# Optimization experiments

Hardware: AMD Instinct MI355X
Metric: run time of the kernel (lower is better)

The kernel has to match this reference:

```python
import jax, jax.numpy as jnp
import numpy as np

B, L, D_MODEL, H, D_QKV = 4, 2048, 1024, 16, 64
SCALE = float(D_MODEL) ** 0.5  # note: source scales by sqrt(d_model), not sqrt(d_qkv)


def setup_inputs() -> dict:
    key = jax.random.key(0)
    ks = jax.random.split(key, 6)
    xavier_qkv = (2.0 / (D_MODEL + D_QKV)) ** 0.5
    xavier_fc = (2.0 / (H * D_QKV + D_MODEL)) ** 0.5
    return {
        "x": jax.random.normal(ks[0], (B, L, D_MODEL), dtype=jnp.float32),
        "mask": jnp.ones((B, L), dtype=jnp.int32),
        "w_q": jax.random.normal(ks[1], (H, D_MODEL, D_QKV), dtype=jnp.float32) * xavier_qkv,
        "w_k": jax.random.normal(ks[2], (H, D_MODEL, D_QKV), dtype=jnp.float32) * xavier_qkv,
        "w_v": jax.random.normal(ks[3], (H, D_MODEL, D_QKV), dtype=jnp.float32) * xavier_qkv,
        "fc_w": jax.random.normal(ks[4], (D_MODEL, H * D_QKV), dtype=jnp.float32) * xavier_fc,
        "fc_b": jnp.zeros((D_MODEL,), dtype=jnp.float32),
    }


def reference(x, mask, w_q, w_k, w_v, fc_w, fc_b):
    # x: [B, L, M]; per-head projections via einsum, as in the source
    q = jnp.einsum('blm,hmd->blhd', x, w_q)
    k = jnp.einsum('blm,hmd->blhd', x, w_k)
    v = jnp.einsum('blm,hmd->blhd', x, w_v)
    scores = jnp.einsum('blhd,bkhd->bhlk', q, k)  # [B, H, L, L]
    m = mask[:, None, None, :]  # unsqueeze(1).unsqueeze(2)
    scores = jnp.where(m == 0, jnp.asarray(-1e9, scores.dtype), scores)
    logits = jax.nn.softmax(scores / SCALE, axis=3)
    # Faithful to source einsum 'bhlk,blhd->blhd' (k is summed out of logits only)
    out = jnp.einsum('bhlk,blhd->blhd', logits, v)
    out = out.reshape(x.shape[0], x.shape[1], H * D_QKV)
    return out @ fc_w.T + fc_b
```

## Files before the change

### kernel.cpp

```cpp
#include <hip/hip_runtime.h>
#include <hip/hip_bf16.h>


typedef __attribute__((ext_vector_type(8))) short bf16x8;
typedef __attribute__((ext_vector_type(4))) float f32x4;

__device__ __forceinline__ f32x4 mfma16(bf16x8 a, bf16x8 b, f32x4 c) {
  return __builtin_amdgcn_mfma_f32_16x16x32_bf16(a, b, c, 0, 0, 0);
}

__device__ __forceinline__ unsigned short f2b(float f) {
  unsigned int u = __builtin_bit_cast(unsigned int, f);
  return (unsigned short)((u + 0x7fffu + ((u >> 16) & 1u)) >> 16);
}

__device__ __forceinline__ bf16x8 cvt8(float4 a, float4 b) {
  bf16x8 r;
  r[0] = (short)f2b(a.x); r[1] = (short)f2b(a.y); r[2] = (short)f2b(a.z); r[3] = (short)f2b(a.w);
  r[4] = (short)f2b(b.x); r[5] = (short)f2b(b.y); r[6] = (short)f2b(b.z); r[7] = (short)f2b(b.w);
  return r;
}

__device__ __forceinline__ void gld_lds16(const void* g, void* l) {
  __builtin_amdgcn_global_load_lds((const __attribute__((address_space(1))) unsigned int*)g,
                                   (__attribute__((address_space(3))) unsigned int*)l, 16, 0, 0);
}

__global__ __launch_bounds__(256) void prep(const float* __restrict__ x,
                                            const float* __restrict__ wv,
                                            const float* __restrict__ fcw,
                                            unsigned short* __restrict__ xb,
                                            unsigned short* __restrict__ wcT) {
  int bid = blockIdx.x, t = threadIdx.x;
  int wid = t >> 6, lane = t & 63, l16 = lane & 15, quad = lane >> 4;

  if (bid < 256) {
    int wr = wid >> 1, wc = wid & 1;
    int row0 = (bid >> 4) * 64 + wr * 32;
    int col0 = (bid & 15) * 64 + wc * 32;
    f32x4 acc[2][2];
#pragma unroll
    for (int a = 0; a < 2; a++)
#pragma unroll
      for (int b = 0; b < 2; b++) acc[a][b] = (f32x4){0.f, 0.f, 0.f, 0.f};

    float4 A0[2][2], B0[2][2];
#define LOADK(kk, Ad, Bd)                                                            \
    {                                                                                \
      int h_ = (kk) >> 6, d_ = (kk) & 63;                                            \
      _Pragma("unroll")                                                              \
      for (int rt = 0; rt < 2; rt++) {                                               \
        const float* pa = fcw + (row0 + rt * 16 + l16) * 1024 + (kk);                \
        Ad[rt][0] = *reinterpret_cast<const float4*>(pa);                            \
        Ad[rt][1] = *reinterpret_cast<const float4*>(pa + 4);                        \
      }                                                                              \
      _Pragma("unroll")                                                              \
      for (int ct = 0; ct < 2; ct++) {                                               \
        const float* pb = wv + h_ * 65536 + (col0 + ct * 16 + l16) * 64 + d_;        \
        Bd[ct][0] = *reinterpret_cast<const float4*>(pb);                            \
        Bd[ct][1] = *reinterpret_cast<const float4*>(pb + 4);                        \
      }                                                                              \
    }
    LOADK(quad * 8, A0, B0);
    for (int k0 = 0; k0 < 1024; k0 += 32) {
      float4 A1[2][2], B1[2][2];
      if (k0 < 992) LOADK(k0 + 32 + quad * 8, A1, B1);
      bf16x8 af[2], bfr[2];
#pragma unroll
      for (int rt = 0; rt < 2; rt++) af[rt] = cvt8(A0[rt][0], A0[rt][1]);
#pragma unroll
      for (int ct = 0; ct < 2; ct++) bfr[ct] = cvt8(B0[ct][0], B0[ct][1]);
#pragma unroll
      for (int rt = 0; rt < 2; rt++)
#pragma unroll
        for (int ct = 0; ct < 2; ct++) acc[rt][ct] = mfma16(af[rt], bfr[ct], acc[rt][ct]);
#pragma unroll
      for (int a = 0; a < 2; a++)
#pragma unroll
        for (int b = 0; b < 2; b++) { A0[a][b] = A1[a][b]; B0[a][b] = B1[a][b]; }
    }
#undef LOADK
#pragma unroll
    for (int rt = 0; rt < 2; rt++)
#pragma unroll
      for (int ct = 0; ct < 2; ct++) {
        int j0 = row0 + rt * 16 + quad * 4;
        int m = col0 + ct * 16 + l16;
#pragma unroll
        for (int r = 0; r < 4; r++) wcT[(j0 + r) * 1024 + m] = f2b(acc[rt][ct][r]);
      }
  } else {
    int base0 = (bid - 256) << 15;
#pragma unroll
    for (int i = 0; i < 16; i++) {
      int idx = base0 + i * 2048 + t * 8;
      float4 a = *reinterpret_cast<const float4*>(x + idx);
      float4 b = *reinterpret_cast<const float4*>(x + idx + 4);
      *reinterpret_cast<bf16x8*>(xb + idx) = cvt8(a, b);
    }
  }
}

__global__ __launch_bounds__(256, 4) void final_gemm(const unsigned short* __restrict__ xb,
                                                     const unsigned short* __restrict__ wcT,
                                                     const float* __restrict__ fcb,
                                                     float* __restrict__ out) {
  __shared__ __align__(16) unsigned short As[2 * 128 * 32];
  __shared__ __align__(16) unsigned short Bs[2 * 64 * 32];
  int t = threadIdx.x, wid = t >> 6, lane = t & 63, l16 = lane & 15, quad = lane >> 4;
  int wr = wid >> 1, wc = wid & 1;
  int row0 = (blockIdx.x >> 4) * 128;
  int col0 = (blockIdx.x & 15) * 64;

  int w4 = wid * 4, w2 = wid * 2;
  const unsigned short* Ap[4];
  const unsigned short* Bp[2];
#pragma unroll
  for (int j = 0; j < 4; j++) {
    int blk = w4 + j, s = blk >> 3;
    int row = (blk & 7) * 16 + (lane >> 2), kq = lane & 3;
    Ap[j] = xb + (row0 + row) * 1024 + s * 32 + kq * 8;
  }
#pragma unroll
  for (int j = 0; j < 2; j++) {
    int blk = w2 + j, s = blk >> 2;
    int row = (blk & 3) * 16 + (lane >> 2), kq = lane & 3;
    Bp[j] = wcT + (col0 + row) * 1024 + s * 32 + kq * 8;
  }

  f32x4 acc[4][2];
#pragma unroll
  for (int rt = 0; rt < 4; rt++)
#pragma unroll
    for (int ct = 0; ct < 2; ct++) acc[rt][ct] = (f32x4){0.f, 0.f, 0.f, 0.f};

  for (int k0 = 0; k0 < 1024; k0 += 64) {
    __syncthreads();
#pragma unroll
    for (int j = 0; j < 4; j++) gld_lds16(Ap[j] + k0, &As[(w4 + j) * 512 + lane * 8]);
#pragma unroll
    for (int j = 0; j < 2; j++) gld_lds16(Bp[j] + k0, &Bs[(w2 + j) * 512 + lane * 8]);
    __syncthreads();
#pragma unroll
    for (int s = 0; s < 2; s++) {
      bf16x8 af[4], bfr[2];
#pragma unroll
      for (int rt = 0; rt < 4; rt++)
        af[rt] = *reinterpret_cast<const bf16x8*>(&As[s * 4096 + (wr * 64 + rt * 16 + l16) * 32 + quad * 8]);
#pragma unroll
      for (int ct = 0; ct < 2; ct++)
        bfr[ct] = *reinterpret_cast<const bf16x8*>(&Bs[s * 2048 + (wc * 32 + ct * 16 + l16) * 32 + quad * 8]);
#pragma unroll
      for (int rt = 0; rt < 4; rt++)
#pragma unroll
        for (int ct = 0; ct < 2; ct++)
          acc[rt][ct] = mfma16(af[rt], bfr[ct], acc[rt][ct]);
    }
  }

#pragma unroll
  for (int ct = 0; ct < 2; ct++) {
    int j = col0 + wc * 32 + ct * 16 + l16;
    float bias = fcb[j];
#pragma unroll
    for (int rt = 0; rt < 4; rt++) {
      int i0 = row0 + wr * 64 + rt * 16 + quad * 4;
      f32x4 a = acc[rt][ct];
#pragma unroll
      for (int r = 0; r < 4; r++) out[(i0 + r) * 1024 + j] = a[r] + bias;
    }
  }
}

extern "C" void kernel_launch(void* const* d_in, const int* in_sizes, int n_in,
                              void* d_out, int out_size, void* d_ws, size_t ws_size,
                              hipStream_t stream) {
  const float* x   = (const float*)d_in[0];
  const float* wv  = (const float*)d_in[4];
  const float* fcw = (const float*)d_in[5];
  const float* fcb = (const float*)d_in[6];
  float* out = (float*)d_out;

  char* ws = (char*)d_ws;
  unsigned short* xb  = (unsigned short*)(ws);
  unsigned short* wcT = (unsigned short*)(ws + 16777216);

  prep<<<512, 256, 0, stream>>>(x, wv, fcw, xb, wcT);
  final_gemm<<<1024, 256, 0, stream>>>(xb, wcT, fcb, out);
}
```

Before: 151.1 us.

## Stage weight-fold GEMM tiles through swizzled LDS and widen conversion grid

After: 133.5 us. -11.6%, faster.

```diff
diff --git a/kernel.cpp b/kernel.cpp
--- a/kernel.cpp
+++ b/kernel.cpp
@@ -31,69 +31,100 @@
                                             const float* __restrict__ fcw,
                                             unsigned short* __restrict__ xb,
                                             unsigned short* __restrict__ wcT) {
+  __shared__ __align__(16) short As[2][64 * 64];
+  __shared__ __align__(16) short Bs[2][64 * 64];
+
   int bid = blockIdx.x, t = threadIdx.x;
   int wid = t >> 6, lane = t & 63, l16 = lane & 15, quad = lane >> 4;
 
   if (bid < 256) {
+    int j0 = (bid >> 4) * 64;
+    int m0 = (bid & 15) * 64;
     int wr = wid >> 1, wc = wid & 1;
-    int row0 = (bid >> 4) * 64 + wr * 32;
-    int col0 = (bid & 15) * 64 + wc * 32;
+    int rowt = t >> 3, colb = (t & 7) * 8;
+
     f32x4 acc[2][2];
 #pragma unroll
     for (int a = 0; a < 2; a++)
 #pragma unroll
       for (int b = 0; b < 2; b++) acc[a][b] = (f32x4){0.f, 0.f, 0.f, 0.f};
 
-    float4 A0[2][2], B0[2][2];
-#define LOADK(kk, Ad, Bd)                                                            \
+    float4 ra[2][2], rb[2][2];
+
+#define LOADH(h)                                                                     \
     {                                                                                \
-      int h_ = (kk) >> 6, d_ = (kk) & 63;                                            \
       _Pragma("unroll")                                                              \
-      for (int rt = 0; rt < 2; rt++) {                                               \
-        const float* pa = fcw + (row0 + rt * 16 + l16) * 1024 + (kk);                \
-        Ad[rt][0] = *reinterpret_cast<const float4*>(pa);                            \
-        Ad[rt][1] = *reinterpret_cast<const float4*>(pa + 4);                        \
+      for (int c = 0; c < 2; c++) {                                                  \
+        int row = c * 32 + rowt;                                                     \
+        const float* pa = fcw + (j0 + row) * 1024 + (h) * 64 + colb;                 \
+        ra[c][0] = *reinterpret_cast<const float4*>(pa);                             \
+        ra[c][1] = *reinterpret_cast<const float4*>(pa + 4);                         \
+        const float* pb = wv + (h) * 65536 + (m0 + row) * 64 + colb;                 \
+        rb[c][0] = *reinterpret_cast<const float4*>(pb);                             \
+        rb[c][1] = *reinterpret_cast<const float4*>(pb + 4);                         \
       }                                                                              \
+    }
+#define STOREH(buf)                                                                  \
+    {                                                                                \
       _Pragma("unroll")                                                              \
-      for (int ct = 0; ct < 2; ct++) {                                               \
-        const float* pb = wv + h_ * 65536 + (col0 + ct * 16 + l16) * 64 + d_;        \
-        Bd[ct][0] = *reinterpret_cast<const float4*>(pb);                            \
-        Bd[ct][1] = *reinterpret_cast<const float4*>(pb + 4);                        \
+      for (int c = 0; c < 2; c++) {                                                  \
+        int row = c * 32 + rowt;                                                     \
+        int bo = row * 128 + ((colb * 2) ^ ((row & 7) << 4));                        \
+        *reinterpret_cast<bf16x8*>((char*)As[buf] + bo) = cvt8(ra[c][0], ra[c][1]);  \
+        *reinterpret_cast<bf16x8*>((char*)Bs[buf] + bo) = cvt8(rb[c][0], rb[c][1]);  \
       }                                                                              \
     }
-    LOADK(quad * 8, A0, B0);
-    for (int k0 = 0; k0 < 1024; k0 += 32) {
-      float4 A1[2][2], B1[2][2];
-      if (k0 < 992) LOADK(k0 + 32 + quad * 8, A1, B1);
-      bf16x8 af[2], bfr[2];
-#pragma unroll
-      for (int rt = 0; rt < 2; rt++) af[rt] = cvt8(A0[rt][0], A0[rt][1]);
-#pragma unroll
-      for (int ct = 0; ct < 2; ct++) bfr[ct] = cvt8(B0[ct][0], B0[ct][1]);
-#pragma unroll
-      for (int rt = 0; rt < 2; rt++)
-#pragma unroll
-        for (int ct = 0; ct < 2; ct++) acc[rt][ct] = mfma16(af[rt], bfr[ct], acc[rt][ct]);
-#pragma unroll
-      for (int a = 0; a < 2; a++)
-#pragma unroll
-        for (int b = 0; b < 2; b++) { A0[a][b] = A1[a][b]; B0[a][b] = B1[a][b]; }
-    }
-#undef LOADK
+
+    LOADH(0);
+    STOREH(0);
+    __syncthreads();
+
+    for (int h = 0; h < 16; ++h) {
+      int cur = h & 1;
+      if (h < 15) LOADH(h + 1);
+
+      bf16x8 af[2][2], bg[2][2];
+#pragma unroll
+      for (int rt = 0; rt < 2; rt++) {
+        int rowf = wr * 32 + rt * 16 + l16;
+        int rbase = rowf * 128, rx = (rowf & 7) << 4;
+        af[rt][0] = *reinterpret_cast<const bf16x8*>((char*)As[cur] + rbase + ((quad * 16) ^ rx));
+        af[rt][1] = *reinterpret_cast<const bf16x8*>((char*)As[cur] + rbase + ((64 + quad * 16) ^ rx));
+      }
+#pragma unroll
+      for (int ct = 0; ct < 2; ct++) {
+        int rowf = wc * 32 + ct * 16 + l16;
+        int rbase = rowf * 128, rx = (rowf & 7) << 4;
+        bg[ct][0] = *reinterpret_cast<const bf16x8*>((char*)Bs[cur] + rbase + ((quad * 16) ^ rx));
+        bg[ct][1] = *reinterpret_cast<const bf16x8*>((char*)Bs[cur] + rbase + ((64 + quad * 16) ^ rx));
+      }
+#pragma unroll
+      for (int ks = 0; ks < 2; ks++)
+#pragma unroll
+        for (int rt = 0; rt < 2; rt++)
+#pragma unroll
+          for (int ct = 0; ct < 2; ct++)
+            acc[rt][ct] = mfma16(af[rt][ks], bg[ct][ks], acc[rt][ct]);
+
+      if (h < 15) STOREH(cur ^ 1);
+      __syncthreads();
+    }
+#undef LOADH
+#undef STOREH
+
 #pragma unroll
     for (int rt = 0; rt < 2; rt++)
 #pragma unroll
       for (int ct = 0; ct < 2; ct++) {
-        int j0 = row0 + rt * 16 + quad * 4;
-        int m = col0 + ct * 16 + l16;
-#pragma unroll
-        for (int r = 0; r < 4; r++) wcT[(j0 + r) * 1024 + m] = f2b(acc[rt][ct][r]);
+        int jj = j0 + wr * 32 + rt * 16 + quad * 4;
+        int mm = m0 + wc * 32 + ct * 16 + l16;
+#pragma unroll
+        for (int r = 0; r < 4; r++) wcT[(jj + r) * 1024 + mm] = f2b(acc[rt][ct][r]);
       }
   } else {
-    int base0 = (bid - 256) << 15;
-#pragma unroll
-    for (int i = 0; i < 16; i++) {
-      int idx = base0 + i * 2048 + t * 8;
+    int cb = bid - 256;
+    for (int ch = cb; ch < 4096; ch += 768) {
+      int idx = ch * 2048 + t * 8;
       float4 a = *reinterpret_cast<const float4*>(x + idx);
       float4 b = *reinterpret_cast<const float4*>(x + idx + 4);
       *reinterpret_cast<bf16x8*>(xb + idx) = cvt8(a, b);
@@ -185,6 +216,6 @@
   unsigned short* xb  = (unsigned short*)(ws);
   unsigned short* wcT = (unsigned short*)(ws + 16777216);
 
-  prep<<<512, 256, 0, stream>>>(x, wv, fcw, xb, wcT);
+  prep<<<1024, 256, 0, stream>>>(x, wv, fcw, xb, wcT);
   final_gemm<<<1024, 256, 0, stream>>>(xb, wcT, fcb, out);
 }
```
